# Kernel tuning notes

Measured on AMD Instinct MI355X. Metric: run time of the kernel, lower is better.

Reference implementation:

```python
import jax, jax.numpy as jnp
import numpy as np

N = 20000   # nodes per graph
E = 320000  # edges (avg degree 16)
B = 2       # batch of graphs
D = 64      # hidden_dim
L = 25      # message-passing layers
EPS = 1e-5


def setup_inputs() -> dict:
    key = jax.random.key(0)
    ks = jax.random.split(key, 12)
    rn = lambda k, s, sc=0.05: jax.random.normal(k, s, dtype=jnp.float32) * sc
    return {
        "x_batch": jax.random.normal(ks[0], (B, N, 3), dtype=jnp.float32),
        "edge_index": jax.random.randint(ks[1], (2, E), 0, N, dtype=jnp.int32),
        "edge_attr": jax.random.normal(ks[2], (E, 2), dtype=jnp.float32),
        "enc_w": rn(ks[3], (3, D)), "enc_b": jnp.zeros((D,), jnp.float32),
        "msg_w1": rn(ks[4], (L, 2 * D + 2, D)), "msg_b1": jnp.zeros((L, D), jnp.float32),
        "msg_ln_g": jnp.ones((L, D), jnp.float32), "msg_ln_b": jnp.zeros((L, D), jnp.float32),
        "msg_w2": rn(ks[5], (L, D, D)), "msg_b2": jnp.zeros((L, D), jnp.float32),
        "up_w": rn(ks[6], (L, 2 * D, D)), "up_b": jnp.zeros((L, D), jnp.float32),
        "up_ln_g": jnp.ones((L, D), jnp.float32), "up_ln_b": jnp.zeros((L, D), jnp.float32),
        "dec_w1": rn(ks[7], (D, 32)), "dec_b1": jnp.zeros((32,), jnp.float32),
        "dec_w2": rn(ks[8], (32, 2)), "dec_b2": jnp.zeros((2,), jnp.float32),
    }


def _ln(x, g, b):
    mu = jnp.mean(x, axis=-1, keepdims=True)
    var = jnp.mean(jnp.square(x - mu), axis=-1, keepdims=True)
    return (x - mu) * jax.lax.rsqrt(var + EPS) * g + b


def reference(x_batch, edge_index, edge_attr,
              enc_w, enc_b,
              msg_w1, msg_b1, msg_ln_g, msg_ln_b, msg_w2, msg_b2,
              up_w, up_b, up_ln_g, up_ln_b,
              dec_w1, dec_b1, dec_w2, dec_b2):
    row, col = edge_index[0], edge_index[1]
    layer_params = (msg_w1, msg_b1, msg_ln_g, msg_ln_b, msg_w2, msg_b2,
                    up_w, up_b, up_ln_g, up_ln_b)

    def step(h, p):  # h: [N, D]
        w1, b1, g1, be1, w2, b2, uw, ub, ug, ube = p
        cat = jnp.concatenate([h[row], h[col], edge_attr], axis=1)  # [E, 2D+2]
        m = jax.nn.relu(_ln(cat @ w1 + b1, g1, be1)) @ w2 + b2      # [E, D]
        aggr = jax.ops.segment_sum(m, row, num_segments=N)          # [N, D]
        u = jax.nn.relu(_ln(jnp.concatenate([h, aggr], axis=1) @ uw + ub, ug, ube))
        return h + u, None

    def graph(x):  # x: [N, 3]
        h0 = x @ enc_w + enc_b
        h, _ = jax.lax.scan(step, h0, layer_params)
        return jax.nn.relu(h @ dec_w1 + dec_b1) @ dec_w2 + dec_b2  # [N, 2]

    return jax.vmap(graph)(x_batch)  # [B, N, 2]
```

## Files before the change

### kernel.cpp

```cpp
#include <hip/hip_runtime.h>

constexpr int N = 20000;
constexpr int E = 320000;
constexpr int Bc = 2;
constexpr int D = 64;
constexpr int L = 25;
constexpr float EPS = 1e-5f;

typedef __attribute__((ext_vector_type(8))) short short8;
typedef __attribute__((ext_vector_type(4))) float f32x4;

__device__ __forceinline__ unsigned short f2bf(float f) {
  unsigned u = __float_as_uint(f);
  u += 0x7fff + ((u >> 16) & 1);
  return (unsigned short)(u >> 16);
}

__global__ void hist_kernel(const int* __restrict__ row, int* __restrict__ deg) {
  int e = blockIdx.x * blockDim.x + threadIdx.x;
  if (e < E) atomicAdd(&deg[row[e]], 1);
}

__global__ __launch_bounds__(1024) void scan_kernel(const int* __restrict__ deg,
                                                    int* __restrict__ row_start,
                                                    int* __restrict__ cursor) {
  __shared__ int s[1024];
  const int t = threadIdx.x;
  constexpr int CH = (N + 1023) / 1024;
  int base = t * CH;
  int sum = 0;
  for (int k = 0; k < CH; ++k) {
    int idx = base + k;
    if (idx < N) sum += deg[idx];
  }
  s[t] = sum;
  __syncthreads();
  for (int off = 1; off < 1024; off <<= 1) {
    int v = (t >= off) ? s[t - off] : 0;
    __syncthreads();
    s[t] += v;
    __syncthreads();
  }
  int excl = s[t] - sum;
  for (int k = 0; k < CH; ++k) {
    int idx = base + k;
    if (idx < N) {
      row_start[idx] = excl;
      cursor[idx] = excl;
      excl += deg[idx];
    }
  }
  if (t == 1023) row_start[N] = s[1023];
}

__global__ void scatter_kernel(const int* __restrict__ row, int* __restrict__ cursor,
                               int* __restrict__ edge_order) {
  int e = blockIdx.x * blockDim.x + threadIdx.x;
  if (e < E) {
    int p = atomicAdd(&cursor[row[e]], 1);
    edge_order[p] = e;
  }
}

__global__ void sortmap_kernel(const int* __restrict__ edge_order,
                               const int* __restrict__ col,
                               const float* __restrict__ eattr,
                               int* __restrict__ col_s, float2* __restrict__ ea_s) {
  int p = blockIdx.x * blockDim.x + threadIdx.x;
  if (p < E) {
    int eid = edge_order[p];
    col_s[p] = col[eid];
    ea_s[p] = *(const float2*)&eattr[2 * (size_t)eid];
  }
}

__global__ __launch_bounds__(512) void encoder_kernel(
    const float* __restrict__ x, const float* __restrict__ enc_w,
    const float* __restrict__ enc_b, float* __restrict__ h,
    unsigned short* __restrict__ hbf) {
  int idx = blockIdx.x * blockDim.x + threadIdx.x;
  if (idx >= Bc * N * D) return;
  int j = idx & (D - 1);
  int bn = idx >> 6;
  const float* xp = x + (size_t)bn * 3;
  float v = enc_b[j] + xp[0] * enc_w[j] + xp[1] * enc_w[D + j] + xp[2] * enc_w[2 * D + j];
  h[idx] = v;
  hbf[idx] = f2bf(v);
}

constexpr int GPN = 8;
constexpr int GPG = N / GPN;
constexpr int NGRP = GPG * Bc;
constexpr int EWB = 8;
constexpr int ETPB = EWB * 64;

__global__ __launch_bounds__(ETPB, 4) void edge_kernel(
    const unsigned short* __restrict__ hbf, float* __restrict__ aggr,
    const int* __restrict__ col_s, const float2* __restrict__ ea_s,
    const int* __restrict__ row_start,
    const float* __restrict__ w1, const float* __restrict__ b1,
    const float* __restrict__ g1, const float* __restrict__ be1,
    const float* __restrict__ w2, const float* __restrict__ b2) {
  __shared__ __align__(16) char smem[40960];
  unsigned short* w1f = (unsigned short*)smem;
  unsigned short* w2f = (unsigned short*)(smem + 16384);
  const int tid = threadIdx.x, lane = tid & 63, w = tid >> 6;
  const int cl = lane & 15, hg = lane >> 4;
  char* pw = smem + 24576 + w * 2048;

  for (int idx = tid; idx < 16 * 512; idx += ETPB) {
    int f = idx >> 9, rem = idx & 511, ln = rem >> 3, i = rem & 7;
    int nt = f >> 2, ks = f & 3;
    int k = ks * 32 + (ln >> 4) * 8 + i, n = nt * 16 + (ln & 15);
    w1f[idx] = f2bf(w1[k * 64 + n]);
  }
  for (int idx = tid; idx < 8 * 512; idx += ETPB) {
    int f = idx >> 9, rem = idx & 511, ln = rem >> 3, i = rem & 7;
    int nt = f >> 1, ks = f & 1;
    int k = ks * 32 + (ln >> 4) * 8 + i, n = nt * 16 + (ln & 15);
    w2f[idx] = f2bf(w2[k * 64 + n]);
  }
  __syncthreads();

  float b1c[4], g1c[4], be1c[4], b2c[4], wA[4], wB[4];
#pragma unroll
  for (int nt = 0; nt < 4; ++nt) {
    int c = nt * 16 + cl;
    b1c[nt] = b1[c]; g1c[nt] = g1[c]; be1c[nt] = be1[c]; b2c[nt] = b2[c];
    wA[nt] = w1[128 * 64 + c]; wB[nt] = w1[129 * 64 + c];
  }
  const short8* w1v = (const short8*)w1f;
  const short8* w2v = (const short8*)w2f;

  const int gw = __builtin_amdgcn_readfirstlane(blockIdx.x * EWB + w);
  const int g = (gw >= GPG) ? 1 : 0;
  const int nb = (gw - g * GPG) * GPN;
  const unsigned short* hb = hbf + (size_t)g * N * 64;
  float* ag = aggr + (size_t)g * N * 64;

  int rs[GPN + 1];
#pragma unroll
  for (int k = 0; k <= GPN; ++k) rs[k] = row_start[nb + k];

  for (int k = 0; k < GPN; ++k) {
    const int es = rs[k], ee = rs[k + 1];
    const int deg = ee - es;
    float macc[4] = {0.f, 0.f, 0.f, 0.f};

    if (deg > 0) {
      const unsigned short* pn = hb + (((size_t)(nb + k)) << 6) + hg * 8;
      const short8 av0 = *(const short8*)pn;
      const short8 av1 = *(const short8*)(pn + 32);

      int pos = es + cl; if (pos >= ee) pos = ee - 1;
      float2 eaC = ea_s[pos];
      const unsigned short* pc0 = hb + (((size_t)col_s[pos]) << 6) + hg * 8;
      short8 a2C = *(const short8*)pc0;
      short8 a3C = *(const short8*)(pc0 + 32);

      for (int ts = es; ts < ee; ts += 16) {
        const bool hasN = (ts + 16) < ee;
        float2 eaN; short8 a2N, a3N;
        if (hasN) {
          int p2 = ts + 16 + cl; if (p2 >= ee) p2 = ee - 1;
          eaN = ea_s[p2];
          const unsigned short* pc = hb + (((size_t)col_s[p2]) << 6) + hg * 8;
          a2N = *(const short8*)pc;
          a3N = *(const short8*)(pc + 32);
        }

        f32x4 acc[4];
#pragma unroll
        for (int nt = 0; nt < 4; ++nt) acc[nt] = (f32x4){0.f, 0.f, 0.f, 0.f};
#pragma unroll
        for (int nt = 0; nt < 4; ++nt)
          acc[nt] = __builtin_amdgcn_mfma_f32_16x16x32_bf16(av0, w1v[(nt * 4 + 0) * 64 + lane], acc[nt], 0, 0, 0);
#pragma unroll
        for (int nt = 0; nt < 4; ++nt)
          acc[nt] = __builtin_amdgcn_mfma_f32_16x16x32_bf16(av1, w1v[(nt * 4 + 1) * 64 + lane], acc[nt], 0, 0, 0);
#pragma unroll
        for (int nt = 0; nt < 4; ++nt)
          acc[nt] = __builtin_amdgcn_mfma_f32_16x16x32_bf16(a2C, w1v[(nt * 4 + 2) * 64 + lane], acc[nt], 0, 0, 0);
#pragma unroll
        for (int nt = 0; nt < 4; ++nt)
          acc[nt] = __builtin_amdgcn_mfma_f32_16x16x32_bf16(a3C, w1v[(nt * 4 + 3) * 64 + lane], acc[nt], 0, 0, 0);

#pragma unroll
        for (int r = 0; r < 4; ++r) {
          const int edge = hg * 4 + r;
          float e0 = __shfl(eaC.x, edge, 64);
          float e1 = __shfl(eaC.y, edge, 64);
          float v[4];
#pragma unroll
          for (int nt = 0; nt < 4; ++nt)
            v[nt] = acc[nt][r] + b1c[nt] + e0 * wA[nt] + e1 * wB[nt];
          float sum = v[0] + v[1] + v[2] + v[3];
#pragma unroll
          for (int o = 1; o < 16; o <<= 1) sum += __shfl_xor(sum, o, 64);
          float mu = sum * (1.f / 64.f);
          float q = 0.f;
#pragma unroll
          for (int nt = 0; nt < 4; ++nt) { v[nt] -= mu; q += v[nt] * v[nt]; }
#pragma unroll
          for (int o = 1; o < 16; o <<= 1) q += __shfl_xor(q, o, 64);
          float rsq = rsqrtf(q * (1.f / 64.f) + EPS);
#pragma unroll
          for (int nt = 0; nt < 4; ++nt) {
            float p = fmaxf(v[nt] * rsq * g1c[nt] + be1c[nt], 0.f);
            unsigned byteoff = (unsigned)(edge * 128 + (nt * 16 + cl) * 2) ^ (unsigned)(hg << 5);
            *(unsigned short*)(pw + byteoff) = f2bf(p);
          }
        }

        f32x4 m[4];
#pragma unroll
        for (int nt = 0; nt < 4; ++nt) m[nt] = (f32x4){0.f, 0.f, 0.f, 0.f};
#pragma unroll
        for (int ks = 0; ks < 2; ++ks) {
          unsigned byteoff = (unsigned)(cl * 128 + (ks * 32 + hg * 8) * 2) ^ (unsigned)((cl >> 2) << 5);
          short8 a2 = *(const short8*)(pw + byteoff);
#pragma unroll
          for (int nt = 0; nt < 4; ++nt)
            m[nt] = __builtin_amdgcn_mfma_f32_16x16x32_bf16(
                a2, w2v[(nt * 2 + ks) * 64 + lane], m[nt], 0, 0, 0);
        }

        const int vleft = ee - ts - hg * 4;
#pragma unroll
        for (int r = 0; r < 4; ++r) {
          if (r < vleft) {
#pragma unroll
            for (int nt = 0; nt < 4; ++nt) macc[nt] += m[nt][r];
          }
        }

        if (hasN) { eaC = eaN; a2C = a2N; a3C = a3N; }
      }
    }

    float fin[4];
#pragma unroll
    for (int nt = 0; nt < 4; ++nt) {
      float s = macc[nt];
      s += __shfl_xor(s, 16, 64);
      s += __shfl_xor(s, 32, 64);
      fin[nt] = s + (float)deg * b2c[nt];
    }
    float sv = (hg == 0) ? fin[0] : (hg == 1) ? fin[1] : (hg == 2) ? fin[2] : fin[3];
    ag[(((size_t)(nb + k)) << 6) + hg * 16 + cl] = sv;
  }
}

constexpr int NT_TOT = Bc * N / 16;
constexpr int NWB = 8;
constexpr int NTPB = 512;

__global__ __launch_bounds__(NTPB) void node_kernel(
    float* __restrict__ h, unsigned short* __restrict__ hbf,
    const float* __restrict__ aggr,
    const float* __restrict__ uw, const float* __restrict__ ub,
    const float* __restrict__ ug, const float* __restrict__ ube) {
  __shared__ __align__(16) unsigned short uwf[16 * 512];

  const int tid = threadIdx.x, lane = tid & 63, w = tid >> 6;
  const int cl = lane & 15, hg = lane >> 4;

  for (int idx = tid; idx < 16 * 512; idx += NTPB) {
    int f = idx >> 9, rem = idx & 511, ln = rem >> 3, i = rem & 7;
    int nt = f >> 2, ks = f & 3;
    int k = ks * 32 + (ln >> 4) * 8 + i, n = nt * 16 + (ln & 15);
    uwf[idx] = f2bf(uw[k * 64 + n]);
  }
  __syncthreads();

  const int tt = blockIdx.x * NWB + w;
  if (tt >= NT_TOT) return;

  float ubc[4], ugc[4], ubec[4];
#pragma unroll
  for (int nt = 0; nt < 4; ++nt) {
    int c = nt * 16 + cl;
    ubc[nt] = ub[c]; ugc[nt] = ug[c]; ubec[nt] = ube[c];
  }
  const short8* uwv = (const short8*)uwf;

  constexpr int TPGn = N / 16;
  const int g = (tt >= TPGn) ? 1 : 0;
  const int nbase = (tt - g * TPGn) * 16;
  const size_t gb = (size_t)g * N * 64;

  const unsigned short* ph = hbf + gb + (((size_t)(nbase + cl)) << 6) + hg * 8;
  short8 av[4];
  av[0] = *(const short8*)ph;
  av[1] = *(const short8*)(ph + 32);
  const float* pa = aggr + gb + (((size_t)(nbase + cl)) << 6) + hg * 8;
  float4 f0 = *(const float4*)pa;
  float4 f1 = *(const float4*)(pa + 4);
  float4 f2 = *(const float4*)(pa + 32);
  float4 f3 = *(const float4*)(pa + 36);
  {
    union { short8 s; unsigned short u[8]; } t2, t3;
    t2.u[0] = f2bf(f0.x); t2.u[1] = f2bf(f0.y); t2.u[2] = f2bf(f0.z); t2.u[3] = f2bf(f0.w);
    t2.u[4] = f2bf(f1.x); t2.u[5] = f2bf(f1.y); t2.u[6] = f2bf(f1.z); t2.u[7] = f2bf(f1.w);
    t3.u[0] = f2bf(f2.x); t3.u[1] = f2bf(f2.y); t3.u[2] = f2bf(f2.z); t3.u[3] = f2bf(f2.w);
    t3.u[4] = f2bf(f3.x); t3.u[5] = f2bf(f3.y); t3.u[6] = f2bf(f3.z); t3.u[7] = f2bf(f3.w);
    av[2] = t2.s; av[3] = t3.s;
  }

  f32x4 acc[4];
#pragma unroll
  for (int nt = 0; nt < 4; ++nt) acc[nt] = (f32x4){0.f, 0.f, 0.f, 0.f};
#pragma unroll
  for (int ks = 0; ks < 4; ++ks) {
#pragma unroll
    for (int nt = 0; nt < 4; ++nt)
      acc[nt] = __builtin_amdgcn_mfma_f32_16x16x32_bf16(
          av[ks], uwv[(nt * 4 + ks) * 64 + lane], acc[nt], 0, 0, 0);
  }

#pragma unroll
  for (int r = 0; r < 4; ++r) {
    float v[4];
#pragma unroll
    for (int nt = 0; nt < 4; ++nt) v[nt] = acc[nt][r] + ubc[nt];
    float sum = v[0] + v[1] + v[2] + v[3];
#pragma unroll
    for (int o = 1; o < 16; o <<= 1) sum += __shfl_xor(sum, o, 64);
    float mu = sum * (1.f / 64.f);
    float q = 0.f;
#pragma unroll
    for (int nt = 0; nt < 4; ++nt) { v[nt] -= mu; q += v[nt] * v[nt]; }
#pragma unroll
    for (int o = 1; o < 16; o <<= 1) q += __shfl_xor(q, o, 64);
    float rs = rsqrtf(q * (1.f / 64.f) + EPS);
    const size_t nrow = gb + (((size_t)(nbase + hg * 4 + r)) << 6);
#pragma unroll
    for (int nt = 0; nt < 4; ++nt) {
      int c = nt * 16 + cl;
      float u = fmaxf(v[nt] * rs * ugc[nt] + ubec[nt], 0.f);
      float nv = h[nrow + c] + u;
      h[nrow + c] = nv;
      hbf[nrow + c] = f2bf(nv);
    }
  }
}

__global__ __launch_bounds__(512) void decoder_kernel(
    const float* __restrict__ h,
    const float* __restrict__ dw1, const float* __restrict__ db1,
    const float* __restrict__ dw2, const float* __restrict__ db2,
    float* __restrict__ out) {
  __shared__ __align__(16) float w1s[64 * 32];
  __shared__ float w2s[64];
  __shared__ float b1s[32];
  __shared__ float hs[8][64];
  const int tid = threadIdx.x;
  const int lane = tid & 63;
  const int w = tid >> 6;

  for (int idx = tid; idx < 64 * 32; idx += 512) w1s[idx] = dw1[idx];
  if (tid < 64) w2s[tid] = dw2[tid];
  if (tid < 32) b1s[tid] = db1[tid];
  const float ob0 = db2[0], ob1 = db2[1];
  __syncthreads();

  const int total = Bc * N;
  const int per_iter = gridDim.x * 8;
  const int niter = (total + per_iter - 1) / per_iter;
  const int wave_global = blockIdx.x * 8 + w;

  for (int it = 0; it < niter; ++it) {
    const int i = it * per_iter + wave_global;
    if (i < total) {
      hs[w][lane] = h[((size_t)i << 6) + lane];
      float s1 = 0.f;
      if (lane < 32) {
        s1 = b1s[lane];
        for (int k = 0; k < 64; ++k) s1 = fmaf(hs[w][k], w1s[k * 32 + lane], s1);
        s1 = fmaxf(s1, 0.f);
      }
      float c0 = (lane < 32) ? s1 * w2s[lane * 2]     : 0.f;
      float c1 = (lane < 32) ? s1 * w2s[lane * 2 + 1] : 0.f;
#pragma unroll
      for (int off = 16; off > 0; off >>= 1) {
        c0 += __shfl_xor(c0, off, 64);
        c1 += __shfl_xor(c1, off, 64);
      }
      if (lane == 0) {
        out[(size_t)i * 2]     = c0 + ob0;
        out[(size_t)i * 2 + 1] = c1 + ob1;
      }
    }
  }
}

extern "C" void kernel_launch(void* const* d_in, const int* in_sizes, int n_in,
                              void* d_out, int out_size, void* d_ws, size_t ws_size,
                              hipStream_t stream) {
  const float* x        = (const float*)d_in[0];
  const int*   ei       = (const int*)d_in[1];
  const float* eattr    = (const float*)d_in[2];
  const float* enc_w    = (const float*)d_in[3];
  const float* enc_b    = (const float*)d_in[4];
  const float* msg_w1   = (const float*)d_in[5];
  const float* msg_b1   = (const float*)d_in[6];
  const float* msg_ln_g = (const float*)d_in[7];
  const float* msg_ln_b = (const float*)d_in[8];
  const float* msg_w2   = (const float*)d_in[9];
  const float* msg_b2   = (const float*)d_in[10];
  const float* up_w     = (const float*)d_in[11];
  const float* up_b     = (const float*)d_in[12];
  const float* up_ln_g  = (const float*)d_in[13];
  const float* up_ln_b  = (const float*)d_in[14];
  const float* dw1      = (const float*)d_in[15];
  const float* db1      = (const float*)d_in[16];
  const float* dw2      = (const float*)d_in[17];
  const float* db2      = (const float*)d_in[18];
  float* out = (float*)d_out;

  float* h            = (float*)d_ws;
  unsigned short* hbf = (unsigned short*)(h + (size_t)Bc * N * D);
  float* aggr         = (float*)(hbf + (size_t)Bc * N * D);
  int* deg        = (int*)(aggr + (size_t)Bc * N * D);
  int* row_start  = deg + N;
  int* cursor     = row_start + N + 1;
  int* edge_order = cursor + N;
  int* col_sv     = edge_order + E;
  float2* ea_sv   = (float2*)(col_sv + E + (E & 1));

  const int* row = ei;
  const int* col = ei + E;

  hipMemsetAsync(deg, 0, N * sizeof(int), stream);
  hist_kernel<<<(E + 255) / 256, 256, 0, stream>>>(row, deg);
  scan_kernel<<<1, 1024, 0, stream>>>(deg, row_start, cursor);
  scatter_kernel<<<(E + 255) / 256, 256, 0, stream>>>(row, cursor, edge_order);
  sortmap_kernel<<<(E + 255) / 256, 256, 0, stream>>>(edge_order, col, eattr, col_sv, ea_sv);
  encoder_kernel<<<(Bc * N * D + 511) / 512, 512, 0, stream>>>(x, enc_w, enc_b, h, hbf);

  for (int l = 0; l < L; ++l) {
    edge_kernel<<<NGRP / EWB, ETPB, 0, stream>>>(
        hbf, aggr, col_sv, ea_sv, row_start,
        msg_w1 + (size_t)l * 130 * 64, msg_b1 + l * 64,
        msg_ln_g + l * 64, msg_ln_b + l * 64,
        msg_w2 + (size_t)l * 64 * 64, msg_b2 + l * 64);
    node_kernel<<<(NT_TOT + NWB - 1) / NWB, NTPB, 0, stream>>>(
        h, hbf, aggr,
        up_w + (size_t)l * 128 * 64, up_b + l * 64,
        up_ln_g + l * 64, up_ln_b + l * 64);
  }

  decoder_kernel<<<512, 512, 0, stream>>>(h, dw1, db1, dw2, db2, out);
}
```

Measured before the change: 2.767 ms.

## Flatten edge-kernel node loop into one software-pipelined tile stream

Reworks the per-wave edge processing so that tiles across all 8 nodes of a group form one continuous stream, prefetching the next tile (including the next node's features) while the current tile computes. Empty-degree nodes get zeroed up front. Edge attributes are now loaded per row directly instead of being broadcast by shuffles. The block size halves to 4 waves, which shrinks LDS per block and may raise occupancy. In exchange the loop control is more complex and uses more registers.

```diff
diff --git a/kernel.cpp b/kernel.cpp
--- a/kernel.cpp
+++ b/kernel.cpp
@@ -91,7 +91,7 @@
 constexpr int GPN = 8;
 constexpr int GPG = N / GPN;
 constexpr int NGRP = GPG * Bc;
-constexpr int EWB = 8;
+constexpr int EWB = 4;
 constexpr int ETPB = EWB * 64;
 
 __global__ __launch_bounds__(ETPB, 4) void edge_kernel(
@@ -101,7 +101,7 @@
     const float* __restrict__ w1, const float* __restrict__ b1,
     const float* __restrict__ g1, const float* __restrict__ be1,
     const float* __restrict__ w2, const float* __restrict__ b2) {
-  __shared__ __align__(16) char smem[40960];
+  __shared__ __align__(16) char smem[24576 + EWB * 2048];
   unsigned short* w1f = (unsigned short*)smem;
   unsigned short* w2f = (unsigned short*)(smem + 16384);
   const int tid = threadIdx.x, lane = tid & 63, w = tid >> 6;
@@ -142,112 +142,139 @@
 #pragma unroll
   for (int k = 0; k <= GPN; ++k) rs[k] = row_start[nb + k];
 
-  for (int k = 0; k < GPN; ++k) {
-    const int es = rs[k], ee = rs[k + 1];
-    const int deg = ee - es;
-    float macc[4] = {0.f, 0.f, 0.f, 0.f};
-
-    if (deg > 0) {
-      const unsigned short* pn = hb + (((size_t)(nb + k)) << 6) + hg * 8;
-      const short8 av0 = *(const short8*)pn;
-      const short8 av1 = *(const short8*)(pn + 32);
-
-      int pos = es + cl; if (pos >= ee) pos = ee - 1;
-      float2 eaC = ea_s[pos];
-      const unsigned short* pc0 = hb + (((size_t)col_s[pos]) << 6) + hg * 8;
-      short8 a2C = *(const short8*)pc0;
-      short8 a3C = *(const short8*)(pc0 + 32);
-
-      for (int ts = es; ts < ee; ts += 16) {
-        const bool hasN = (ts + 16) < ee;
-        float2 eaN; short8 a2N, a3N;
-        if (hasN) {
-          int p2 = ts + 16 + cl; if (p2 >= ee) p2 = ee - 1;
-          eaN = ea_s[p2];
-          const unsigned short* pc = hb + (((size_t)col_s[p2]) << 6) + hg * 8;
-          a2N = *(const short8*)pc;
-          a3N = *(const short8*)(pc + 32);
-        }
-
-        f32x4 acc[4];
-#pragma unroll
-        for (int nt = 0; nt < 4; ++nt) acc[nt] = (f32x4){0.f, 0.f, 0.f, 0.f};
-#pragma unroll
-        for (int nt = 0; nt < 4; ++nt)
-          acc[nt] = __builtin_amdgcn_mfma_f32_16x16x32_bf16(av0, w1v[(nt * 4 + 0) * 64 + lane], acc[nt], 0, 0, 0);
-#pragma unroll
-        for (int nt = 0; nt < 4; ++nt)
-          acc[nt] = __builtin_amdgcn_mfma_f32_16x16x32_bf16(av1, w1v[(nt * 4 + 1) * 64 + lane], acc[nt], 0, 0, 0);
-#pragma unroll
-        for (int nt = 0; nt < 4; ++nt)
-          acc[nt] = __builtin_amdgcn_mfma_f32_16x16x32_bf16(a2C, w1v[(nt * 4 + 2) * 64 + lane], acc[nt], 0, 0, 0);
-#pragma unroll
-        for (int nt = 0; nt < 4; ++nt)
-          acc[nt] = __builtin_amdgcn_mfma_f32_16x16x32_bf16(a3C, w1v[(nt * 4 + 3) * 64 + lane], acc[nt], 0, 0, 0);
-
-#pragma unroll
-        for (int r = 0; r < 4; ++r) {
-          const int edge = hg * 4 + r;
-          float e0 = __shfl(eaC.x, edge, 64);
-          float e1 = __shfl(eaC.y, edge, 64);
-          float v[4];
-#pragma unroll
-          for (int nt = 0; nt < 4; ++nt)
-            v[nt] = acc[nt][r] + b1c[nt] + e0 * wA[nt] + e1 * wB[nt];
-          float sum = v[0] + v[1] + v[2] + v[3];
-#pragma unroll
-          for (int o = 1; o < 16; o <<= 1) sum += __shfl_xor(sum, o, 64);
-          float mu = sum * (1.f / 64.f);
-          float q = 0.f;
-#pragma unroll
-          for (int nt = 0; nt < 4; ++nt) { v[nt] -= mu; q += v[nt] * v[nt]; }
-#pragma unroll
-          for (int o = 1; o < 16; o <<= 1) q += __shfl_xor(q, o, 64);
-          float rsq = rsqrtf(q * (1.f / 64.f) + EPS);
-#pragma unroll
-          for (int nt = 0; nt < 4; ++nt) {
-            float p = fmaxf(v[nt] * rsq * g1c[nt] + be1c[nt], 0.f);
-            unsigned byteoff = (unsigned)(edge * 128 + (nt * 16 + cl) * 2) ^ (unsigned)(hg << 5);
-            *(unsigned short*)(pw + byteoff) = f2bf(p);
-          }
-        }
-
-        f32x4 m[4];
-#pragma unroll
-        for (int nt = 0; nt < 4; ++nt) m[nt] = (f32x4){0.f, 0.f, 0.f, 0.f};
-#pragma unroll
-        for (int ks = 0; ks < 2; ++ks) {
-          unsigned byteoff = (unsigned)(cl * 128 + (ks * 32 + hg * 8) * 2) ^ (unsigned)((cl >> 2) << 5);
-          short8 a2 = *(const short8*)(pw + byteoff);
-#pragma unroll
-          for (int nt = 0; nt < 4; ++nt)
-            m[nt] = __builtin_amdgcn_mfma_f32_16x16x32_bf16(
-                a2, w2v[(nt * 2 + ks) * 64 + lane], m[nt], 0, 0, 0);
-        }
-
-        const int vleft = ee - ts - hg * 4;
-#pragma unroll
-        for (int r = 0; r < 4; ++r) {
-          if (r < vleft) {
-#pragma unroll
-            for (int nt = 0; nt < 4; ++nt) macc[nt] += m[nt][r];
-          }
-        }
-
-        if (hasN) { eaC = eaN; a2C = a2N; a3C = a3N; }
-      }
-    }
-
-    float fin[4];
-#pragma unroll
-    for (int nt = 0; nt < 4; ++nt) {
-      float s = macc[nt];
-      s += __shfl_xor(s, 16, 64);
-      s += __shfl_xor(s, 32, 64);
-      fin[nt] = s + (float)deg * b2c[nt];
-    }
-    float sv = (hg == 0) ? fin[0] : (hg == 1) ? fin[1] : (hg == 2) ? fin[2] : fin[3];
-    ag[(((size_t)(nb + k)) << 6) + hg * 16 + cl] = sv;
+#pragma unroll
+  for (int k = 0; k < GPN; ++k)
+    if (rs[k + 1] == rs[k]) ag[(((size_t)(nb + k)) << 6) + lane] = 0.f;
+
+  int kC = 0;
+  while (kC < GPN && rs[kC + 1] == rs[kC]) ++kC;
+  if (kC >= GPN) return;
+  int tsC = rs[kC];
+
+  short8 av0C, av1C, a2C, a3C;
+  float2 eaC0, eaC1, eaC2, eaC3;
+  {
+    const unsigned short* pn = hb + (((size_t)(nb + kC)) << 6) + hg * 8;
+    av0C = *(const short8*)pn; av1C = *(const short8*)(pn + 32);
+    const int ee = rs[kC + 1];
+    int p = tsC + cl; if (p >= ee) p = ee - 1;
+    const unsigned short* pc = hb + (((size_t)col_s[p]) << 6) + hg * 8;
+    a2C = *(const short8*)pc; a3C = *(const short8*)(pc + 32);
+    int p0 = tsC + hg * 4;
+    int q0 = min(p0, ee - 1), q1 = min(p0 + 1, ee - 1), q2 = min(p0 + 2, ee - 1), q3 = min(p0 + 3, ee - 1);
+    eaC0 = ea_s[q0]; eaC1 = ea_s[q1]; eaC2 = ea_s[q2]; eaC3 = ea_s[q3];
+  }
+
+  float macc[4] = {0.f, 0.f, 0.f, 0.f};
+  bool valid = true;
+
+  while (valid) {
+    int kN = kC, tsN = tsC + 16;
+    bool validN = true;
+    if (tsN >= rs[kC + 1]) {
+      kN = kC + 1;
+      while (kN < GPN && rs[kN + 1] == rs[kN]) ++kN;
+      if (kN < GPN) tsN = rs[kN]; else validN = false;
+    }
+
+    short8 av0N, av1N, a2N, a3N;
+    float2 eaN0, eaN1, eaN2, eaN3;
+    if (validN) {
+      const int ee = rs[kN + 1];
+      int p = tsN + cl; if (p >= ee) p = ee - 1;
+      const unsigned short* pc = hb + (((size_t)col_s[p]) << 6) + hg * 8;
+      a2N = *(const short8*)pc; a3N = *(const short8*)(pc + 32);
+      int p0 = tsN + hg * 4;
+      int q0 = min(p0, ee - 1), q1 = min(p0 + 1, ee - 1), q2 = min(p0 + 2, ee - 1), q3 = min(p0 + 3, ee - 1);
+      eaN0 = ea_s[q0]; eaN1 = ea_s[q1]; eaN2 = ea_s[q2]; eaN3 = ea_s[q3];
+      if (kN != kC) {
+        const unsigned short* pn = hb + (((size_t)(nb + kN)) << 6) + hg * 8;
+        av0N = *(const short8*)pn; av1N = *(const short8*)(pn + 32);
+      } else { av0N = av0C; av1N = av1C; }
+    }
+
+    f32x4 acc[4];
+#pragma unroll
+    for (int nt = 0; nt < 4; ++nt) acc[nt] = (f32x4){0.f, 0.f, 0.f, 0.f};
+#pragma unroll
+    for (int nt = 0; nt < 4; ++nt)
+      acc[nt] = __builtin_amdgcn_mfma_f32_16x16x32_bf16(av0C, w1v[(nt * 4 + 0) * 64 + lane], acc[nt], 0, 0, 0);
+#pragma unroll
+    for (int nt = 0; nt < 4; ++nt)
+      acc[nt] = __builtin_amdgcn_mfma_f32_16x16x32_bf16(av1C, w1v[(nt * 4 + 1) * 64 + lane], acc[nt], 0, 0, 0);
+#pragma unroll
+    for (int nt = 0; nt < 4; ++nt)
+      acc[nt] = __builtin_amdgcn_mfma_f32_16x16x32_bf16(a2C, w1v[(nt * 4 + 2) * 64 + lane], acc[nt], 0, 0, 0);
+#pragma unroll
+    for (int nt = 0; nt < 4; ++nt)
+      acc[nt] = __builtin_amdgcn_mfma_f32_16x16x32_bf16(a3C, w1v[(nt * 4 + 3) * 64 + lane], acc[nt], 0, 0, 0);
+
+#pragma unroll
+    for (int r = 0; r < 4; ++r) {
+      const int edge = hg * 4 + r;
+      const float2 ea = (r == 0) ? eaC0 : (r == 1) ? eaC1 : (r == 2) ? eaC2 : eaC3;
+      float v[4];
+#pragma unroll
+      for (int nt = 0; nt < 4; ++nt)
+        v[nt] = acc[nt][r] + b1c[nt] + ea.x * wA[nt] + ea.y * wB[nt];
+      float sum = v[0] + v[1] + v[2] + v[3];
+#pragma unroll
+      for (int o = 1; o < 16; o <<= 1) sum += __shfl_xor(sum, o, 64);
+      float mu = sum * (1.f / 64.f);
+      float q = 0.f;
+#pragma unroll
+      for (int nt = 0; nt < 4; ++nt) { v[nt] -= mu; q += v[nt] * v[nt]; }
+#pragma unroll
+      for (int o = 1; o < 16; o <<= 1) q += __shfl_xor(q, o, 64);
+      float rsq = rsqrtf(q * (1.f / 64.f) + EPS);
+#pragma unroll
+      for (int nt = 0; nt < 4; ++nt) {
+        float p = fmaxf(v[nt] * rsq * g1c[nt] + be1c[nt], 0.f);
+        unsigned byteoff = (unsigned)(edge * 128 + (nt * 16 + cl) * 2) ^ (unsigned)(hg << 5);
+        *(unsigned short*)(pw + byteoff) = f2bf(p);
+      }
+    }
+
+    f32x4 m[4];
+#pragma unroll
+    for (int nt = 0; nt < 4; ++nt) m[nt] = (f32x4){0.f, 0.f, 0.f, 0.f};
+#pragma unroll
+    for (int ks = 0; ks < 2; ++ks) {
+      unsigned byteoff = (unsigned)(cl * 128 + (ks * 32 + hg * 8) * 2) ^ (unsigned)((cl >> 2) << 5);
+      short8 a2 = *(const short8*)(pw + byteoff);
+#pragma unroll
+      for (int nt = 0; nt < 4; ++nt)
+        m[nt] = __builtin_amdgcn_mfma_f32_16x16x32_bf16(
+            a2, w2v[(nt * 2 + ks) * 64 + lane], m[nt], 0, 0, 0);
+    }
+
+    const int vleft = rs[kC + 1] - tsC - hg * 4;
+#pragma unroll
+    for (int r = 0; r < 4; ++r) {
+      if (r < vleft) {
+#pragma unroll
+        for (int nt = 0; nt < 4; ++nt) macc[nt] += m[nt][r];
+      }
+    }
+
+    if (!validN || kN != kC) {
+      const int deg = rs[kC + 1] - rs[kC];
+      float fin[4];
+#pragma unroll
+      for (int nt = 0; nt < 4; ++nt) {
+        float s = macc[nt];
+        s += __shfl_xor(s, 16, 64);
+        s += __shfl_xor(s, 32, 64);
+        fin[nt] = s + (float)deg * b2c[nt];
+        macc[nt] = 0.f;
+      }
+      float sv = (hg == 0) ? fin[0] : (hg == 1) ? fin[1] : (hg == 2) ? fin[2] : fin[3];
+      ag[(((size_t)(nb + kC)) << 6) + hg * 16 + cl] = sv;
+    }
+
+    kC = kN; tsC = tsN; valid = validN;
+    av0C = av0N; av1C = av1N; a2C = a2N; a3C = a3N;
+    eaC0 = eaN0; eaC1 = eaN1; eaC2 = eaN2; eaC3 = eaN3;
   }
 }
 
@@ -423,10 +450,10 @@
   float* aggr         = (float*)(hbf + (size_t)Bc * N * D);
   int* deg        = (int*)(aggr + (size_t)Bc * N * D);
   int* row_start  = deg + N;
-  int* cursor     = row_start + N + 1;
+  int* cursor     = row_start + N + 4;
   int* edge_order = cursor + N;
   int* col_sv     = edge_order + E;
-  float2* ea_sv   = (float2*)(col_sv + E + (E & 1));
+  float2* ea_sv   = (float2*)(col_sv + E);
 
   const int* row = ei;
   const int* col = ei + E;
```

Result: slower. 3.205 ms (+15.8%).

## Fuse edge and node update kernels into one per-layer kernel with ping-pong bf16 buffers

Applied to the files above, without the earlier changes.

Merges the edge message kernel and the node update kernel into a single layer kernel. Each wave keeps its node group's aggregated messages in LDS and runs the update MLP and LayerNorm right away, so the fp32 aggr array is never written to or read back from global memory. A second bf16 hidden buffer is alternated between layers so neighbours can still read the old state while the new one is written. The nodes per wave drop from 8 to 4, which doubles the wave count. The update MFMA is now only a quarter utilized (4 valid rows out of 16), each block converts the extra update weights into LDS, and LDS use per block rises. Both LayerNorms also switch to a single-pass mean and variance.

```diff
diff --git a/kernel.cpp b/kernel.cpp
--- a/kernel.cpp
+++ b/kernel.cpp
@@ -88,31 +88,38 @@
   hbf[idx] = f2bf(v);
 }
 
-constexpr int GPN = 8;
+constexpr int GPN = 4;
 constexpr int GPG = N / GPN;
 constexpr int NGRP = GPG * Bc;
 constexpr int EWB = 8;
 constexpr int ETPB = EWB * 64;
 
-__global__ __launch_bounds__(ETPB, 4) void edge_kernel(
-    const unsigned short* __restrict__ hbf, float* __restrict__ aggr,
+__global__ __launch_bounds__(ETPB, 4) void layer_kernel(
+    const unsigned short* __restrict__ hbf_old, unsigned short* __restrict__ hbf_new,
+    float* __restrict__ h,
     const int* __restrict__ col_s, const float2* __restrict__ ea_s,
     const int* __restrict__ row_start,
     const float* __restrict__ w1, const float* __restrict__ b1,
     const float* __restrict__ g1, const float* __restrict__ be1,
-    const float* __restrict__ w2, const float* __restrict__ b2) {
-  __shared__ __align__(16) char smem[40960];
+    const float* __restrict__ w2, const float* __restrict__ b2,
+    const float* __restrict__ uw, const float* __restrict__ ub,
+    const float* __restrict__ ug, const float* __restrict__ ube) {
+  __shared__ __align__(16) char smem[40960 + EWB * 3072];
   unsigned short* w1f = (unsigned short*)smem;
   unsigned short* w2f = (unsigned short*)(smem + 16384);
+  unsigned short* uwf = (unsigned short*)(smem + 24576);
+
   const int tid = threadIdx.x, lane = tid & 63, w = tid >> 6;
   const int cl = lane & 15, hg = lane >> 4;
-  char* pw = smem + 24576 + w * 2048;
+  char* pw = smem + 40960 + w * 3072;
+  float* aggs = (float*)(pw + 2048);
 
   for (int idx = tid; idx < 16 * 512; idx += ETPB) {
     int f = idx >> 9, rem = idx & 511, ln = rem >> 3, i = rem & 7;
     int nt = f >> 2, ks = f & 3;
     int k = ks * 32 + (ln >> 4) * 8 + i, n = nt * 16 + (ln & 15);
     w1f[idx] = f2bf(w1[k * 64 + n]);
+    uwf[idx] = f2bf(uw[k * 64 + n]);
   }
   for (int idx = tid; idx < 8 * 512; idx += ETPB) {
     int f = idx >> 9, rem = idx & 511, ln = rem >> 3, i = rem & 7;
@@ -122,120 +129,124 @@
   }
   __syncthreads();
 
-  float b1c[4], g1c[4], be1c[4], b2c[4], wA[4], wB[4];
+  float b1c[4], g1c[4], be1c[4], b2c[4], wA[4], wB[4], ubc[4], ugc[4], ubec[4];
 #pragma unroll
   for (int nt = 0; nt < 4; ++nt) {
     int c = nt * 16 + cl;
     b1c[nt] = b1[c]; g1c[nt] = g1[c]; be1c[nt] = be1[c]; b2c[nt] = b2[c];
     wA[nt] = w1[128 * 64 + c]; wB[nt] = w1[129 * 64 + c];
+    ubc[nt] = ub[c]; ugc[nt] = ug[c]; ubec[nt] = ube[c];
   }
   const short8* w1v = (const short8*)w1f;
   const short8* w2v = (const short8*)w2f;
+  const short8* uwv = (const short8*)uwf;
 
   const int gw = __builtin_amdgcn_readfirstlane(blockIdx.x * EWB + w);
+  if (gw >= NGRP) return;
   const int g = (gw >= GPG) ? 1 : 0;
   const int nb = (gw - g * GPG) * GPN;
-  const unsigned short* hb = hbf + (size_t)g * N * 64;
-  float* ag = aggr + (size_t)g * N * 64;
+  const unsigned short* hb = hbf_old + (size_t)g * N * 64;
 
   int rs[GPN + 1];
 #pragma unroll
   for (int k = 0; k <= GPN; ++k) rs[k] = row_start[nb + k];
+
+#pragma unroll
+  for (int k = 0; k < GPN; ++k) aggs[k * 64 + lane] = 0.f;
 
   for (int k = 0; k < GPN; ++k) {
     const int es = rs[k], ee = rs[k + 1];
     const int deg = ee - es;
+    if (deg == 0) continue;
     float macc[4] = {0.f, 0.f, 0.f, 0.f};
 
-    if (deg > 0) {
-      const unsigned short* pn = hb + (((size_t)(nb + k)) << 6) + hg * 8;
-      const short8 av0 = *(const short8*)pn;
-      const short8 av1 = *(const short8*)(pn + 32);
-
-      int pos = es + cl; if (pos >= ee) pos = ee - 1;
-      float2 eaC = ea_s[pos];
-      const unsigned short* pc0 = hb + (((size_t)col_s[pos]) << 6) + hg * 8;
-      short8 a2C = *(const short8*)pc0;
-      short8 a3C = *(const short8*)(pc0 + 32);
-
-      for (int ts = es; ts < ee; ts += 16) {
-        const bool hasN = (ts + 16) < ee;
-        float2 eaN; short8 a2N, a3N;
-        if (hasN) {
-          int p2 = ts + 16 + cl; if (p2 >= ee) p2 = ee - 1;
-          eaN = ea_s[p2];
-          const unsigned short* pc = hb + (((size_t)col_s[p2]) << 6) + hg * 8;
-          a2N = *(const short8*)pc;
-          a3N = *(const short8*)(pc + 32);
+    const unsigned short* pn = hb + (((size_t)(nb + k)) << 6) + hg * 8;
+    const short8 av0 = *(const short8*)pn;
+    const short8 av1 = *(const short8*)(pn + 32);
+
+    int pos = es + cl; if (pos >= ee) pos = ee - 1;
+    float2 eaC = ea_s[pos];
+    const unsigned short* pc0 = hb + (((size_t)col_s[pos]) << 6) + hg * 8;
+    short8 a2C = *(const short8*)pc0;
+    short8 a3C = *(const short8*)(pc0 + 32);
+
+    for (int ts = es; ts < ee; ts += 16) {
+      const bool hasN = (ts + 16) < ee;
+      float2 eaN; short8 a2N, a3N;
+      if (hasN) {
+        int p2 = ts + 16 + cl; if (p2 >= ee) p2 = ee - 1;
+        eaN = ea_s[p2];
+        const unsigned short* pc = hb + (((size_t)col_s[p2]) << 6) + hg * 8;
+        a2N = *(const short8*)pc;
+        a3N = *(const short8*)(pc + 32);
+      }
+
+      f32x4 acc[4];
+#pragma unroll
+      for (int nt = 0; nt < 4; ++nt) acc[nt] = (f32x4){0.f, 0.f, 0.f, 0.f};
+#pragma unroll
+      for (int nt = 0; nt < 4; ++nt)
+        acc[nt] = __builtin_amdgcn_mfma_f32_16x16x32_bf16(av0, w1v[(nt * 4 + 0) * 64 + lane], acc[nt], 0, 0, 0);
+#pragma unroll
+      for (int nt = 0; nt < 4; ++nt)
+        acc[nt] = __builtin_amdgcn_mfma_f32_16x16x32_bf16(av1, w1v[(nt * 4 + 1) * 64 + lane], acc[nt], 0, 0, 0);
+#pragma unroll
+      for (int nt = 0; nt < 4; ++nt)
+        acc[nt] = __builtin_amdgcn_mfma_f32_16x16x32_bf16(a2C, w1v[(nt * 4 + 2) * 64 + lane], acc[nt], 0, 0, 0);
+#pragma unroll
+      for (int nt = 0; nt < 4; ++nt)
+        acc[nt] = __builtin_amdgcn_mfma_f32_16x16x32_bf16(a3C, w1v[(nt * 4 + 3) * 64 + lane], acc[nt], 0, 0, 0);
+
+#pragma unroll
+      for (int r = 0; r < 4; ++r) {
+        const int edge = hg * 4 + r;
+        float e0 = __shfl(eaC.x, edge, 64);
+        float e1 = __shfl(eaC.y, edge, 64);
+        float v[4];
+#pragma unroll
+        for (int nt = 0; nt < 4; ++nt)
+          v[nt] = acc[nt][r] + b1c[nt] + e0 * wA[nt] + e1 * wB[nt];
+        float s = v[0] + v[1] + v[2] + v[3];
+        float q = v[0] * v[0] + v[1] * v[1] + v[2] * v[2] + v[3] * v[3];
+#pragma unroll
+        for (int o = 1; o < 16; o <<= 1) {
+          s += __shfl_xor(s, o, 64);
+          q += __shfl_xor(q, o, 64);
         }
-
-        f32x4 acc[4];
-#pragma unroll
-        for (int nt = 0; nt < 4; ++nt) acc[nt] = (f32x4){0.f, 0.f, 0.f, 0.f};
+        float mu = s * (1.f / 64.f);
+        float var = fmaf(-mu, mu, q * (1.f / 64.f));
+        float rsq = rsqrtf(var + EPS);
+#pragma unroll
+        for (int nt = 0; nt < 4; ++nt) {
+          float p = fmaxf((v[nt] - mu) * rsq * g1c[nt] + be1c[nt], 0.f);
+          unsigned byteoff = (unsigned)(edge * 128 + (nt * 16 + cl) * 2) ^ (unsigned)(hg << 5);
+          *(unsigned short*)(pw + byteoff) = f2bf(p);
+        }
+      }
+
+      f32x4 m[4];
+#pragma unroll
+      for (int nt = 0; nt < 4; ++nt) m[nt] = (f32x4){0.f, 0.f, 0.f, 0.f};
+#pragma unroll
+      for (int ks = 0; ks < 2; ++ks) {
+        unsigned byteoff = (unsigned)(cl * 128 + (ks * 32 + hg * 8) * 2) ^ (unsigned)((cl >> 2) << 5);
+        short8 a2 = *(const short8*)(pw + byteoff);
 #pragma unroll
         for (int nt = 0; nt < 4; ++nt)
-          acc[nt] = __builtin_amdgcn_mfma_f32_16x16x32_bf16(av0, w1v[(nt * 4 + 0) * 64 + lane], acc[nt], 0, 0, 0);
-#pragma unroll
-        for (int nt = 0; nt < 4; ++nt)
-          acc[nt] = __builtin_amdgcn_mfma_f32_16x16x32_bf16(av1, w1v[(nt * 4 + 1) * 64 + lane], acc[nt], 0, 0, 0);
-#pragma unroll
-        for (int nt = 0; nt < 4; ++nt)
-          acc[nt] = __builtin_amdgcn_mfma_f32_16x16x32_bf16(a2C, w1v[(nt * 4 + 2) * 64 + lane], acc[nt], 0, 0, 0);
-#pragma unroll
-        for (int nt = 0; nt < 4; ++nt)
-          acc[nt] = __builtin_amdgcn_mfma_f32_16x16x32_bf16(a3C, w1v[(nt * 4 + 3) * 64 + lane], acc[nt], 0, 0, 0);
-
-#pragma unroll
-        for (int r = 0; r < 4; ++r) {
-          const int edge = hg * 4 + r;
-          float e0 = __shfl(eaC.x, edge, 64);
-          float e1 = __shfl(eaC.y, edge, 64);
-          float v[4];
-#pragma unroll
-          for (int nt = 0; nt < 4; ++nt)
-            v[nt] = acc[nt][r] + b1c[nt] + e0 * wA[nt] + e1 * wB[nt];
-          float sum = v[0] + v[1] + v[2] + v[3];
-#pragma unroll
-          for (int o = 1; o < 16; o <<= 1) sum += __shfl_xor(sum, o, 64);
-          float mu = sum * (1.f / 64.f);
-          float q = 0.f;
-#pragma unroll
-          for (int nt = 0; nt < 4; ++nt) { v[nt] -= mu; q += v[nt] * v[nt]; }
-#pragma unroll
-          for (int o = 1; o < 16; o <<= 1) q += __shfl_xor(q, o, 64);
-          float rsq = rsqrtf(q * (1.f / 64.f) + EPS);
-#pragma unroll
-          for (int nt = 0; nt < 4; ++nt) {
-            float p = fmaxf(v[nt] * rsq * g1c[nt] + be1c[nt], 0.f);
-            unsigned byteoff = (unsigned)(edge * 128 + (nt * 16 + cl) * 2) ^ (unsigned)(hg << 5);
-            *(unsigned short*)(pw + byteoff) = f2bf(p);
-          }
+          m[nt] = __builtin_amdgcn_mfma_f32_16x16x32_bf16(
+              a2, w2v[(nt * 2 + ks) * 64 + lane], m[nt], 0, 0, 0);
+      }
+
+      const int vleft = ee - ts - hg * 4;
+#pragma unroll
+      for (int r = 0; r < 4; ++r) {
+        if (r < vleft) {
+#pragma unroll
+          for (int nt = 0; nt < 4; ++nt) macc[nt] += m[nt][r];
         }
-
-        f32x4 m[4];
-#pragma unroll
-        for (int nt = 0; nt < 4; ++nt) m[nt] = (f32x4){0.f, 0.f, 0.f, 0.f};
-#pragma unroll
-        for (int ks = 0; ks < 2; ++ks) {
-          unsigned byteoff = (unsigned)(cl * 128 + (ks * 32 + hg * 8) * 2) ^ (unsigned)((cl >> 2) << 5);
-          short8 a2 = *(const short8*)(pw + byteoff);
-#pragma unroll
-          for (int nt = 0; nt < 4; ++nt)
-            m[nt] = __builtin_amdgcn_mfma_f32_16x16x32_bf16(
-                a2, w2v[(nt * 2 + ks) * 64 + lane], m[nt], 0, 0, 0);
-        }
-
-        const int vleft = ee - ts - hg * 4;
-#pragma unroll
-        for (int r = 0; r < 4; ++r) {
-          if (r < vleft) {
-#pragma unroll
-            for (int nt = 0; nt < 4; ++nt) macc[nt] += m[nt][r];
-          }
-        }
-
-        if (hasN) { eaC = eaN; a2C = a2N; a3C = a3N; }
-      }
+      }
+
+      if (hasN) { eaC = eaN; a2C = a2N; a3C = a3N; }
     }
 
     float fin[4];
@@ -247,100 +258,67 @@
       fin[nt] = s + (float)deg * b2c[nt];
     }
     float sv = (hg == 0) ? fin[0] : (hg == 1) ? fin[1] : (hg == 2) ? fin[2] : fin[3];
-    ag[(((size_t)(nb + k)) << 6) + hg * 16 + cl] = sv;
-  }
-}
-
-constexpr int NT_TOT = Bc * N / 16;
-constexpr int NWB = 8;
-constexpr int NTPB = 512;
-
-__global__ __launch_bounds__(NTPB) void node_kernel(
-    float* __restrict__ h, unsigned short* __restrict__ hbf,
-    const float* __restrict__ aggr,
-    const float* __restrict__ uw, const float* __restrict__ ub,
-    const float* __restrict__ ug, const float* __restrict__ ube) {
-  __shared__ __align__(16) unsigned short uwf[16 * 512];
-
-  const int tid = threadIdx.x, lane = tid & 63, w = tid >> 6;
-  const int cl = lane & 15, hg = lane >> 4;
-
-  for (int idx = tid; idx < 16 * 512; idx += NTPB) {
-    int f = idx >> 9, rem = idx & 511, ln = rem >> 3, i = rem & 7;
-    int nt = f >> 2, ks = f & 3;
-    int k = ks * 32 + (ln >> 4) * 8 + i, n = nt * 16 + (ln & 15);
-    uwf[idx] = f2bf(uw[k * 64 + n]);
-  }
-  __syncthreads();
-
-  const int tt = blockIdx.x * NWB + w;
-  if (tt >= NT_TOT) return;
-
-  float ubc[4], ugc[4], ubec[4];
-#pragma unroll
-  for (int nt = 0; nt < 4; ++nt) {
-    int c = nt * 16 + cl;
-    ubc[nt] = ub[c]; ugc[nt] = ug[c]; ubec[nt] = ube[c];
-  }
-  const short8* uwv = (const short8*)uwf;
-
-  constexpr int TPGn = N / 16;
-  const int g = (tt >= TPGn) ? 1 : 0;
-  const int nbase = (tt - g * TPGn) * 16;
-  const size_t gb = (size_t)g * N * 64;
-
-  const unsigned short* ph = hbf + gb + (((size_t)(nbase + cl)) << 6) + hg * 8;
-  short8 av[4];
-  av[0] = *(const short8*)ph;
-  av[1] = *(const short8*)(ph + 32);
-  const float* pa = aggr + gb + (((size_t)(nbase + cl)) << 6) + hg * 8;
-  float4 f0 = *(const float4*)pa;
-  float4 f1 = *(const float4*)(pa + 4);
-  float4 f2 = *(const float4*)(pa + 32);
-  float4 f3 = *(const float4*)(pa + 36);
+    aggs[k * 64 + ((hg * 16 + cl) ^ (k << 3))] = sv;
+  }
+
   {
-    union { short8 s; unsigned short u[8]; } t2, t3;
-    t2.u[0] = f2bf(f0.x); t2.u[1] = f2bf(f0.y); t2.u[2] = f2bf(f0.z); t2.u[3] = f2bf(f0.w);
-    t2.u[4] = f2bf(f1.x); t2.u[5] = f2bf(f1.y); t2.u[6] = f2bf(f1.z); t2.u[7] = f2bf(f1.w);
-    t3.u[0] = f2bf(f2.x); t3.u[1] = f2bf(f2.y); t3.u[2] = f2bf(f2.z); t3.u[3] = f2bf(f2.w);
-    t3.u[4] = f2bf(f3.x); t3.u[5] = f2bf(f3.y); t3.u[6] = f2bf(f3.z); t3.u[7] = f2bf(f3.w);
-    av[2] = t2.s; av[3] = t3.s;
-  }
-
-  f32x4 acc[4];
-#pragma unroll
-  for (int nt = 0; nt < 4; ++nt) acc[nt] = (f32x4){0.f, 0.f, 0.f, 0.f};
-#pragma unroll
-  for (int ks = 0; ks < 4; ++ks) {
-#pragma unroll
-    for (int nt = 0; nt < 4; ++nt)
-      acc[nt] = __builtin_amdgcn_mfma_f32_16x16x32_bf16(
-          av[ks], uwv[(nt * 4 + ks) * 64 + lane], acc[nt], 0, 0, 0);
-  }
-
-#pragma unroll
-  for (int r = 0; r < 4; ++r) {
-    float v[4];
-#pragma unroll
-    for (int nt = 0; nt < 4; ++nt) v[nt] = acc[nt][r] + ubc[nt];
-    float sum = v[0] + v[1] + v[2] + v[3];
-#pragma unroll
-    for (int o = 1; o < 16; o <<= 1) sum += __shfl_xor(sum, o, 64);
-    float mu = sum * (1.f / 64.f);
-    float q = 0.f;
-#pragma unroll
-    for (int nt = 0; nt < 4; ++nt) { v[nt] -= mu; q += v[nt] * v[nt]; }
-#pragma unroll
-    for (int o = 1; o < 16; o <<= 1) q += __shfl_xor(q, o, 64);
-    float rs = rsqrtf(q * (1.f / 64.f) + EPS);
-    const size_t nrow = gb + (((size_t)(nbase + hg * 4 + r)) << 6);
-#pragma unroll
-    for (int nt = 0; nt < 4; ++nt) {
-      int c = nt * 16 + cl;
-      float u = fmaxf(v[nt] * rs * ugc[nt] + ubec[nt], 0.f);
-      float nv = h[nrow + c] + u;
-      h[nrow + c] = nv;
-      hbf[nrow + c] = f2bf(nv);
+    const int nc = (cl < GPN) ? cl : (GPN - 1);
+    const unsigned short* ph = hb + (((size_t)(nb + nc)) << 6) + hg * 8;
+    short8 av[4];
+    av[0] = *(const short8*)ph;
+    av[1] = *(const short8*)(ph + 32);
+    const int i0 = nc * 64 + ((hg * 8) ^ (nc << 3));
+    const int i1 = nc * 64 + (((32 + hg * 8)) ^ (nc << 3));
+    float4 q0 = *(const float4*)&aggs[i0];
+    float4 q1 = *(const float4*)&aggs[i0 + 4];
+    float4 q2 = *(const float4*)&aggs[i1];
+    float4 q3 = *(const float4*)&aggs[i1 + 4];
+    {
+      union { short8 s; unsigned short u[8]; } t2, t3;
+      t2.u[0] = f2bf(q0.x); t2.u[1] = f2bf(q0.y); t2.u[2] = f2bf(q0.z); t2.u[3] = f2bf(q0.w);
+      t2.u[4] = f2bf(q1.x); t2.u[5] = f2bf(q1.y); t2.u[6] = f2bf(q1.z); t2.u[7] = f2bf(q1.w);
+      t3.u[0] = f2bf(q2.x); t3.u[1] = f2bf(q2.y); t3.u[2] = f2bf(q2.z); t3.u[3] = f2bf(q2.w);
+      t3.u[4] = f2bf(q3.x); t3.u[5] = f2bf(q3.y); t3.u[6] = f2bf(q3.z); t3.u[7] = f2bf(q3.w);
+      av[2] = t2.s; av[3] = t3.s;
+    }
+
+    f32x4 acc[4];
+#pragma unroll
+    for (int nt = 0; nt < 4; ++nt) acc[nt] = (f32x4){0.f, 0.f, 0.f, 0.f};
+#pragma unroll
+    for (int ks = 0; ks < 4; ++ks) {
+#pragma unroll
+      for (int nt = 0; nt < 4; ++nt)
+        acc[nt] = __builtin_amdgcn_mfma_f32_16x16x32_bf16(
+            av[ks], uwv[(nt * 4 + ks) * 64 + lane], acc[nt], 0, 0, 0);
+    }
+
+#pragma unroll
+    for (int r = 0; r < 4; ++r) {
+      float v[4];
+#pragma unroll
+      for (int nt = 0; nt < 4; ++nt) v[nt] = acc[nt][r] + ubc[nt];
+      float s = v[0] + v[1] + v[2] + v[3];
+      float q = v[0] * v[0] + v[1] * v[1] + v[2] * v[2] + v[3] * v[3];
+#pragma unroll
+      for (int o = 1; o < 16; o <<= 1) {
+        s += __shfl_xor(s, o, 64);
+        q += __shfl_xor(q, o, 64);
+      }
+      float mu = s * (1.f / 64.f);
+      float var = fmaf(-mu, mu, q * (1.f / 64.f));
+      float rsq = rsqrtf(var + EPS);
+      if (hg == 0) {
+        const size_t nrow = ((size_t)(g * N + nb + r)) << 6;
+#pragma unroll
+        for (int nt = 0; nt < 4; ++nt) {
+          int c = nt * 16 + cl;
+          float u = fmaxf((v[nt] - mu) * rsq * ugc[nt] + ubec[nt], 0.f);
+          float nv = h[nrow + c] + u;
+          h[nrow + c] = nv;
+          hbf_new[nrow + c] = f2bf(nv);
+        }
+      }
     }
   }
 }
@@ -418,15 +396,15 @@
   const float* db2      = (const float*)d_in[18];
   float* out = (float*)d_out;
 
-  float* h            = (float*)d_ws;
-  unsigned short* hbf = (unsigned short*)(h + (size_t)Bc * N * D);
-  float* aggr         = (float*)(hbf + (size_t)Bc * N * D);
-  int* deg        = (int*)(aggr + (size_t)Bc * N * D);
-  int* row_start  = deg + N;
-  int* cursor     = row_start + N + 1;
-  int* edge_order = cursor + N;
-  int* col_sv     = edge_order + E;
-  float2* ea_sv   = (float2*)(col_sv + E + (E & 1));
+  float* h             = (float*)d_ws;
+  unsigned short* hbf0 = (unsigned short*)(h + (size_t)Bc * N * D);
+  unsigned short* hbf1 = hbf0 + (size_t)Bc * N * D;
+  float2* ea_sv        = (float2*)(hbf1 + (size_t)Bc * N * D);
+  int* col_sv          = (int*)(ea_sv + E);
+  int* edge_order      = col_sv + E;
+  int* deg             = edge_order + E;
+  int* row_start       = deg + N;
+  int* cursor          = row_start + N + 1;
 
   const int* row = ei;
   const int* col = ei + E;
@@ -436,16 +414,16 @@
   scan_kernel<<<1, 1024, 0, stream>>>(deg, row_start, cursor);
   scatter_kernel<<<(E + 255) / 256, 256, 0, stream>>>(row, cursor, edge_order);
   sortmap_kernel<<<(E + 255) / 256, 256, 0, stream>>>(edge_order, col, eattr, col_sv, ea_sv);
-  encoder_kernel<<<(Bc * N * D + 511) / 512, 512, 0, stream>>>(x, enc_w, enc_b, h, hbf);
-
+  encoder_kernel<<<(Bc * N * D + 511) / 512, 512, 0, stream>>>(x, enc_w, enc_b, h, hbf0);
+
+  unsigned short* hbufs[2] = {hbf0, hbf1};
   for (int l = 0; l < L; ++l) {
-    edge_kernel<<<NGRP / EWB, ETPB, 0, stream>>>(
-        hbf, aggr, col_sv, ea_sv, row_start,
+    layer_kernel<<<NGRP / EWB, ETPB, 0, stream>>>(
+        hbufs[l & 1], hbufs[(l + 1) & 1], h,
+        col_sv, ea_sv, row_start,
         msg_w1 + (size_t)l * 130 * 64, msg_b1 + l * 64,
         msg_ln_g + l * 64, msg_ln_b + l * 64,
-        msg_w2 + (size_t)l * 64 * 64, msg_b2 + l * 64);
-    node_kernel<<<(NT_TOT + NWB - 1) / NWB, NTPB, 0, stream>>>(
-        h, hbf, aggr,
+        msg_w2 + (size_t)l * 64 * 64, msg_b2 + l * 64,
         up_w + (size_t)l * 128 * 64, up_b + l * 64,
         up_ln_g + l * 64, up_ln_b + l * 64);
   }
```

New measurement: 2.514 ms. 1.1x faster.
